# Performance work log

Hardware: AMD Instinct MI355X
Metric: run time of the kernel (lower is better)

## Reference

```python
import jax, jax.numpy as jnp
import numpy as np

B, N, E_PER = 512, 256, 8192          # graphs, nodes per graph, edges per graph
FIN, H, K, FOUT = 128, 32, 16, 10     # in_channels, hidden, num clusters, out_channels
EPS = 1e-15


def setup_inputs() -> dict:
    key = jax.random.key(0)
    ks = jax.random.split(key, 12)
    x = jax.random.normal(ks[0], (B * N, FIN), jnp.float32)
    # intra-graph random edges, then offset into the global node index space
    src = jax.random.randint(ks[1], (B, E_PER), 0, N)
    dst = jax.random.randint(ks[2], (B, E_PER), 0, N)
    offs = (jnp.arange(B) * N)[:, None]
    edge_index = jnp.stack([(src + offs).reshape(-1), (dst + offs).reshape(-1)]).astype(jnp.int64)
    batch = jnp.repeat(jnp.arange(B), N).astype(jnp.int64)

    def lin(k, fin, fout):
        return (jax.random.normal(k, (fin, fout), jnp.float32) / np.sqrt(fin)).astype(jnp.float32)

    params = {
        'W_lin1': lin(ks[3], FIN, H), 'b_lin1': jnp.zeros((H,), jnp.float32),
        'W_rel1': lin(ks[4], H, H), 'b_rel1': jnp.zeros((H,), jnp.float32),
        'W_root1': lin(ks[5], H, H),
        'W_pool': lin(ks[6], H, K), 'b_pool': jnp.zeros((K,), jnp.float32),
        'W_rel2': lin(ks[7], H, H), 'b_rel2': jnp.zeros((H,), jnp.float32),
        'W_root2': lin(ks[8], H, H),
        'W_lin2': lin(ks[9], H, H), 'b_lin2': jnp.zeros((H,), jnp.float32),
        'W_lin3': lin(ks[10], H, FOUT), 'b_lin3': jnp.zeros((FOUT,), jnp.float32),
    }
    return {'x': x, 'edge_index': edge_index, 'batch': batch, **params}


def _densify(x, edge_index, batch):
    """to_dense_adj + to_dense_batch: [total,F] -> [B,N,F], [B,N,N], [B,N]."""
    n_total = x.shape[0]
    counts = jax.ops.segment_sum(jnp.ones((n_total,), jnp.int32), batch, num_segments=B)
    offsets = jnp.concatenate([jnp.zeros((1,), jnp.int32), jnp.cumsum(counts)[:-1]])
    pos = jnp.arange(n_total) - offsets[batch]            # position of node inside its graph
    eb = batch[edge_index[0]]                             # graph id of each edge
    adj = jnp.zeros((B, N, N), jnp.float32).at[eb, pos[edge_index[0]], pos[edge_index[1]]].add(1.0)
    xd = jnp.zeros((B, N, x.shape[1]), jnp.float32).at[batch, pos].set(x)
    mask = jnp.zeros((B, N), jnp.float32).at[batch, pos].set(1.0)
    return xd, adj, mask


def _dense_graph_conv(x, adj, W_rel, b_rel, W_root):
    # PyG DenseGraphConv(aggr='add'): lin_rel(adj @ x) + lin_root(x)
    return jnp.einsum('bnm,bmh,hk->bnk', adj, x, W_rel) + b_rel + x @ W_root


def _dense_mincut_pool(x, adj, s, mask):
    s = jax.nn.softmax(s, axis=-1)
    x = x * mask[..., None]
    s = s * mask[..., None]
    out = jnp.einsum('bnk,bnh->bkh', s, x)                        # s^T x
    out_adj = jnp.einsum('bnk,bnm,bmj->bkj', s, adj, s)           # s^T A s
    mincut_num = jnp.einsum('bkk->b', out_adj)
    d_flat = adj.sum(-1)                                          # degree
    mincut_den = jnp.einsum('bnk,bn,bnk->b', s, d_flat, s)        # trace(s^T D s)
    mincut_loss = jnp.mean(-(mincut_num / mincut_den))
    ss = jnp.einsum('bnk,bnj->bkj', s, s)
    ss_norm = jnp.linalg.norm(ss, axis=(-1, -2), keepdims=True)
    i_s = jnp.eye(K, dtype=jnp.float32)
    ortho_loss = jnp.mean(jnp.linalg.norm(ss / ss_norm - i_s / jnp.sqrt(jnp.float32(K)), axis=(-1, -2)))
    # zero diagonal, symmetric degree normalization
    diag_mask = 1.0 - i_s
    out_adj = out_adj * diag_mask
    d = jnp.sqrt(out_adj.sum(-1))[:, None, :] + EPS               # [B,1,K]
    out_adj = out_adj / d / jnp.swapaxes(d, 1, 2)
    return out, out_adj, mincut_loss, ortho_loss


def reference(x, edge_index, batch, W_lin1, b_lin1, W_rel1, b_rel1, W_root1,
              W_pool, b_pool, W_rel2, b_rel2, W_root2, W_lin2, b_lin2, W_lin3, b_lin3):
    xd, adj, mask = _densify(x, edge_index, batch)
    h = xd @ W_lin1 + b_lin1                                      # lin1
    h = _dense_graph_conv(h, adj, W_rel1, b_rel1, W_root1)        # conv1
    s2 = h @ W_pool + b_pool                                      # pool2
    h, adj_p, mincut_loss2, ortho_loss2 = _dense_mincut_pool(h, adj, s2, mask)
    h = _dense_graph_conv(h, adj_p, W_rel2, b_rel2, W_root2)      # conv2
    h = h.sum(axis=1)                                             # readout sum over clusters
    h = jax.nn.relu(h @ W_lin2 + b_lin2)
    h = h @ W_lin3 + b_lin3
    return jax.nn.log_softmax(h, axis=-1), mincut_loss2, ortho_loss2
```

## Files before the change

### kernel.cpp

```cpp
#include <hip/hip_runtime.h>

#define NB 512
#define NN 256
#define EPG 8192
#define FINC 128

typedef float f32x4 __attribute__((ext_vector_type(4)));
typedef short s16x8 __attribute__((ext_vector_type(8)));

__device__ __forceinline__ float bf2f(unsigned short u) {
  union { unsigned int i; float f; } x; x.i = ((unsigned int)u) << 16; return x.f;
}
__device__ __forceinline__ unsigned short f2bf(float f) {
  union { float f; unsigned int i; } x; x.f = f;
  unsigned int r = x.i + 0x7fffu + ((x.i >> 16) & 1u);
  return (unsigned short)(r >> 16);
}
__device__ __forceinline__ unsigned pk2(unsigned short a, unsigned short c) {
  return (unsigned)a | ((unsigned)c << 16);
}

union U16x8 { uint4 u; s16x8 s; };
__device__ __forceinline__ s16x8 dec8(unsigned d) {
  U16x8 o;
  o.u.x = 0x41804180u | ((d & 0x0000000Fu) << 3)  | ((d & 0x000000F0u) << 15);
  o.u.y = 0x41804180u | ((d & 0x00000F00u) >> 5)  | ((d & 0x0000F000u) << 7);
  o.u.z = 0x41804180u | ((d & 0x000F0000u) >> 13) | ((d & 0x00F00000u) >> 1);
  o.u.w = 0x41804180u | ((d & 0x0F000000u) >> 21) | ((d & 0xF0000000u) >> 9);
  return o.s;
}

struct Params {
  const void* x; const void* ei;
  const void *wl1, *bl1, *wr1, *br1, *wro1, *wp, *bp;
  const void *wr2, *br2, *wro2, *wl2, *bl2, *wl3, *bl3;
  float* out; float* ws;
};

__device__ __forceinline__ float ldf(const void* p, int i, bool bf) {
  return bf ? bf2f(((const unsigned short*)p)[i]) : ((const float*)p)[i];
}

#define SMEM_TOTAL 81920

__global__ __launch_bounds__(1024, 8) void mincut_main(Params P) {
  extern __shared__ char smem[];
  const int t = threadIdx.x;
  const int b = blockIdx.x;

  const int wv = t >> 6, lane = t & 63;
  const int lm = lane & 15, quad = lane >> 4;
  const int mbase = wv * 16;

  int* flg = (int*)(smem + 78656);
  if (wv == 0) {
    const unsigned short* pw = (const unsigned short*)P.wr1;
    unsigned e = (pw[lane] >> 7) & 0xFFu;
    unsigned long long m = __ballot(e > 96u && e < 132u);
    if (lane == 0) flg[0] = (__popcll(m) >= 56) ? 1 : 0;
  } else if (wv == 1) {
    const int* pi = (const int*)P.ei + EPG;
    bool c = false;
    if (lane < 32) { int v = pi[lane]; c = (v >= 256 && v < 512); }
    unsigned long long m = __ballot(c);
    if (lane == 0) flg[1] = (__popcll(m) < 24) ? 1 : 0;
  }

  float* oadjb  = (float*)(smem + 2048);
  float* ddb    = (float*)(smem + 6144);
  float* caf    = (float*)(smem + 6208);
  float* psf    = (float*)(smem + 6272);
  float* qsf    = (float*)(smem + 6400);
  float* rb     = (float*)(smem + 8256);
  float* yb     = (float*)(smem + 8384);
  float* lgb    = (float*)(smem + 8512);
  float* rel2f  = (float*)(smem + 9216);
  float* root2f = (float*)(smem + 13312);
  float* lin2f  = (float*)(smem + 17408);
  float* lin3f  = (float*)(smem + 21504);
  float* brel2f = (float*)(smem + 22784);
  float* blin2f = (float*)(smem + 22912);
  float* blin3f = (float*)(smem + 23040);
  float* pbuf   = (float*)(smem + 24576);
  float* ssA    = (float*)(smem + 30720);
  unsigned short* h0T  = (unsigned short*)(smem + 33792);
  unsigned short* h1Th = (unsigned short*)(smem + 33792);
  unsigned short* w1t  = (unsigned short*)(smem + 50688);
  unsigned short* zT   = (unsigned short*)(smem + 50688);
  unsigned short* sTh  = (unsigned short*)(smem + 50688);
  unsigned short* wrelTh = (unsigned short*)(smem + 67584);
  unsigned short* wrootT = (unsigned short*)(smem + 72704);
  float* blin1f = (float*)(smem + 75264);
  unsigned short* taT = (unsigned short*)(smem + 67584);
  unsigned short* wpoolTh = (unsigned short*)(smem + 76032);
  float*          colzF   = (float*)(smem + 78336);
  float*          colsF   = (float*)(smem + 78464);
  float*          scrE    = (float*)(smem + 78528);
  float*          bpf     = (float*)(smem + 78592);
  unsigned short* brel1h  = (unsigned short*)(smem + 81856);

  {
    uint4 z = {0u, 0u, 0u, 0u};
    for (int i = t; i < 2112; i += 1024) ((uint4*)smem)[i] = z;
  }
  if (t < 48) colzF[t] = 0.f;
  __syncthreads();

  const bool BF  = (flg[0] != 0);
  const bool I64 = (flg[1] != 0);

  uint4 ea0, ea1, ea2, ea3, eb0, eb1, eb2, eb3;
  if (I64) {
    const uint4* s4 = (const uint4*)((const long long*)P.ei + (size_t)b * EPG) + t * 4;
    const uint4* d4 = (const uint4*)((const long long*)P.ei + (size_t)NB * EPG + (size_t)b * EPG) + t * 4;
    ea0 = s4[0]; ea1 = s4[1]; ea2 = s4[2]; ea3 = s4[3];
    eb0 = d4[0]; eb1 = d4[1]; eb2 = d4[2]; eb3 = d4[3];
  } else {
    const uint4* s4 = (const uint4*)((const int*)P.ei + (size_t)b * EPG) + t * 2;
    const uint4* d4 = (const uint4*)((const int*)P.ei + (size_t)NB * EPG + (size_t)b * EPG) + t * 2;
    ea0 = s4[0]; ea1 = s4[1];
    eb0 = d4[0]; eb1 = d4[1];
  }

  for (int e = t; e < 4096; e += 1024) {
    int k = e >> 5, c = e & 31;
    w1t[c * 136 + k] = f2bf(ldf(P.wl1, e, BF));
  }
  {
    int k = t >> 5, c = t & 31;
    wrelTh[c * 40 + k] = f2bf(ldf(P.wr1, t, BF));
    wrootT[c * 40 + k] = f2bf(ldf(P.wro1, t, BF));
  }
  if (t < 512) {
    int m = t >> 4, c = t & 15;
    wpoolTh[c * 36 + m] = f2bf(ldf(P.wp, t, BF));
  }
  if (t < 32) { blin1f[t] = ldf(P.bl1, t, BF); brel1h[t] = f2bf(ldf(P.br1, t, BF)); }
  if (t < 16) bpf[t] = ldf(P.bp, t, BF);

  if (I64) {
    #pragma unroll
    for (int i = 0; i < 4; ++i) {
      uint4 a = (i == 0) ? ea0 : (i == 1) ? ea1 : (i == 2) ? ea2 : ea3;
      uint4 c = (i == 0) ? eb0 : (i == 1) ? eb1 : (i == 2) ? eb2 : eb3;
      unsigned n0 = (a.x & 255u) * 264u + (c.x & 255u);
      unsigned n1 = (a.z & 255u) * 264u + (c.z & 255u);
      atomicAdd((unsigned int*)(smem + ((n0 >> 3) << 2)), 1u << ((n0 & 7u) * 4u));
      atomicAdd((unsigned int*)(smem + ((n1 >> 3) << 2)), 1u << ((n1 & 7u) * 4u));
    }
  } else {
    #pragma unroll
    for (int i = 0; i < 2; ++i) {
      uint4 a = (i == 0) ? ea0 : ea1;
      uint4 c = (i == 0) ? eb0 : eb1;
      unsigned n0 = (a.x & 255u) * 264u + (c.x & 255u);
      unsigned n1 = (a.y & 255u) * 264u + (c.y & 255u);
      unsigned n2 = (a.z & 255u) * 264u + (c.z & 255u);
      unsigned n3 = (a.w & 255u) * 264u + (c.w & 255u);
      atomicAdd((unsigned int*)(smem + ((n0 >> 3) << 2)), 1u << ((n0 & 7u) * 4u));
      atomicAdd((unsigned int*)(smem + ((n1 >> 3) << 2)), 1u << ((n1 & 7u) * 4u));
      atomicAdd((unsigned int*)(smem + ((n2 >> 3) << 2)), 1u << ((n2 & 7u) * 4u));
      atomicAdd((unsigned int*)(smem + ((n3 >> 3) << 2)), 1u << ((n3 & 7u) * 4u));
    }
  }

  s16x8 xa[4];
  {
    const size_t node = (size_t)(b * 256 + mbase + lm);
    if (BF) {
      #pragma unroll
      for (int ks = 0; ks < 4; ++ks)
        xa[ks] = *(const s16x8*)((const unsigned short*)P.x + node * 128 + ks * 32 + quad * 8);
    } else {
      #pragma unroll
      for (int ks = 0; ks < 4; ++ks) {
        const float* xp = (const float*)P.x + node * 128 + ks * 32 + quad * 8;
        f32x4 v0 = *(const f32x4*)xp;
        f32x4 v1 = *(const f32x4*)(xp + 4);
        #pragma unroll
        for (int j = 0; j < 4; ++j) { xa[ks][j] = (short)f2bf(v0[j]); xa[ks][4 + j] = (short)f2bf(v1[j]); }
      }
    }
  }
  __syncthreads();

  {
    f32x4 acc[2] = {{0.f,0.f,0.f,0.f},{0.f,0.f,0.f,0.f}};
    #pragma unroll
    for (int ks = 0; ks < 4; ++ks) {
      const int k0 = ks * 32 + quad * 8;
      #pragma unroll
      for (int ct = 0; ct < 2; ++ct) {
        s16x8 bh = *(const s16x8*)(w1t + (ct * 16 + lm) * 136 + k0);
        acc[ct] = __builtin_amdgcn_mfma_f32_16x16x32_bf16(xa[ks], bh, acc[ct], 0, 0, 0);
      }
    }
    #pragma unroll
    for (int ct = 0; ct < 2; ++ct) {
      const int c = ct * 16 + lm;
      float bias = blin1f[c];
      *(uint2*)(h0T + c * 264 + mbase + quad * 4) =
          make_uint2(pk2(f2bf(acc[ct][0] + bias), f2bf(acc[ct][1] + bias)),
                     pk2(f2bf(acc[ct][2] + bias), f2bf(acc[ct][3] + bias)));
    }
  }
  __syncthreads();

  f32x4 racc[2] = {{0.f,0.f,0.f,0.f},{0.f,0.f,0.f,0.f}};
  {
    s16x8 Ah;
    #pragma unroll
    for (int j = 0; j < 8; ++j) Ah[j] = (short)h0T[(quad * 8 + j) * 264 + mbase + lm];
    f32x4 zacc[2] = {{0.f,0.f,0.f,0.f},{0.f,0.f,0.f,0.f}};
    #pragma unroll
    for (int ct = 0; ct < 2; ++ct) {
      const int c = ct * 16 + lm;
      s16x8 brh = *(const s16x8*)(wrelTh + c * 40 + quad * 8);
      s16x8 bro = *(const s16x8*)(wrootT + c * 40 + quad * 8);
      zacc[ct] = __builtin_amdgcn_mfma_f32_16x16x32_bf16(Ah, brh, zacc[ct], 0, 0, 0);
      racc[ct] = __builtin_amdgcn_mfma_f32_16x16x32_bf16(Ah, bro, racc[ct], 0, 0, 0);
    }
    #pragma unroll
    for (int ct = 0; ct < 2; ++ct) {
      unsigned short u0 = f2bf(zacc[ct][0]), u1 = f2bf(zacc[ct][1]);
      unsigned short u2 = f2bf(zacc[ct][2]), u3 = f2bf(zacc[ct][3]);
      *(uint2*)(zT + (ct * 16 + lm) * 264 + mbase + quad * 4) =
          make_uint2(pk2(u0, u1), pk2(u2, u3));
      float pz = (bf2f(u0) + bf2f(u1)) + (bf2f(u2) + bf2f(u3));
      pz += __shfl_xor(pz, 16, 64);
      pz += __shfl_xor(pz, 32, 64);
      if (lane < 16) atomicAdd(colzF + ct * 16 + lm, pz);
    }
  }
  __syncthreads();

  float degf;
  {
    f32x4 h1acc[2] = { racc[0], racc[1] };
    unsigned dsum = 0;
    const char* arow = smem + (mbase + lm) * 132;
    #pragma unroll
    for (int ks = 0; ks < 8; ++ks) {
      unsigned d = *(const unsigned int*)(arow + ks * 16 + quad * 4);
      unsigned v = (d & 0x0F0F0F0Fu) + ((d >> 4) & 0x0F0F0F0Fu);
      dsum += (v * 0x01010101u) >> 24;
      s16x8 af = dec8(d);
      const int v0 = ks * 32 + quad * 8;
      #pragma unroll
      for (int ct = 0; ct < 2; ++ct) {
        s16x8 bz = *(const s16x8*)(zT + (ct * 16 + lm) * 264 + v0);
        h1acc[ct] = __builtin_amdgcn_mfma_f32_16x16x32_bf16(af, bz, h1acc[ct], 0, 0, 0);
      }
    }
    dsum += __shfl_xor(dsum, 16, 64);
    dsum += __shfl_xor(dsum, 32, 64);
    degf = (float)dsum;
    #pragma unroll
    for (int ct = 0; ct < 2; ++ct) {
      const int c = ct * 16 + lm;
      float bias = bf2f(brel1h[c]) - 16.f * colzF[c];
      *(uint2*)(h1Th + c * 264 + mbase + quad * 4) =
          make_uint2(pk2(f2bf(h1acc[ct][0] + bias), f2bf(h1acc[ct][1] + bias)),
                     pk2(f2bf(h1acc[ct][2] + bias), f2bf(h1acc[ct][3] + bias)));
    }
  }
  __syncthreads();

  {
    s16x8 Ah1;
    #pragma unroll
    for (int j = 0; j < 8; ++j) Ah1[j] = (short)h1Th[(quad * 8 + j) * 264 + mbase + lm];
    s16x8 Bh;
    ((uint2*)&Bh)[0] = *(const uint2*)(wpoolTh + lm * 36 + quad * 8);
    ((uint2*)&Bh)[1] = *(const uint2*)(wpoolTh + lm * 36 + quad * 8 + 4);
    f32x4 lacc = {0.f, 0.f, 0.f, 0.f};
    lacc = __builtin_amdgcn_mfma_f32_16x16x32_bf16(Ah1, Bh, lacc, 0, 0, 0);
    f32x4 lg;
    float bm = bpf[lm];
    #pragma unroll
    for (int r = 0; r < 4; ++r) lg[r] = lacc[r] + bm;
    f32x4 mx = lg;
    #pragma unroll
    for (int m = 1; m <= 8; m <<= 1)
      #pragma unroll
      for (int r = 0; r < 4; ++r) mx[r] = fmaxf(mx[r], __shfl_xor(mx[r], m, 64));
    #pragma unroll
    for (int r = 0; r < 4; ++r) lg[r] = __expf(lg[r] - mx[r]);
    f32x4 sm = lg;
    #pragma unroll
    for (int m = 1; m <= 8; m <<= 1)
      #pragma unroll
      for (int r = 0; r < 4; ++r) sm[r] += __shfl_xor(sm[r], m, 64);
    f32x4 sval, sq;
    #pragma unroll
    for (int r = 0; r < 4; ++r) { sval[r] = lg[r] / sm[r]; sq[r] = sval[r] * sval[r]; }
    #pragma unroll
    for (int m = 1; m <= 8; m <<= 1)
      #pragma unroll
      for (int r = 0; r < 4; ++r) sq[r] += __shfl_xor(sq[r], m, 64);
    {
      unsigned short h0s = f2bf(sval[0]);
      unsigned short h1s = f2bf(sval[1]);
      unsigned short h2s = f2bf(sval[2]);
      unsigned short h3s = f2bf(sval[3]);
      const int nb = lm * 264 + mbase + quad * 4;
      *(uint2*)(sTh + nb) = make_uint2(pk2(h0s, h1s), pk2(h2s, h3s));
      float sr = (bf2f(h0s) + bf2f(h1s)) + (bf2f(h2s) + bf2f(h3s));
      sr += __shfl_xor(sr, 16, 64);
      sr += __shfl_xor(sr, 32, 64);
      if (lane < 16) atomicAdd(colsF + lm, sr);
    }
    {
      int l = lane & 15, src = (l >> 2) << 4;
      float q0 = __shfl(sq[0], src, 64), q1 = __shfl(sq[1], src, 64);
      float q2 = __shfl(sq[2], src, 64), q3 = __shfl(sq[3], src, 64);
      float ssel = (l & 2) ? ((l & 1) ? q3 : q2) : ((l & 1) ? q1 : q0);
      float vden = (lane < 16) ? degf * ssel : 0.f;
      #pragma unroll
      for (int o = 32; o > 0; o >>= 1) vden += __shfl_xor(vden, o, 64);
      if (lane == 0) scrE[wv] = vden;
    }
  }
  __syncthreads();

  {
    float cols = colsF[lm];
    f32x4 tacc = {0.f, 0.f, 0.f, 0.f};
    const char* arow = smem + (mbase + lm) * 132;
    #pragma unroll
    for (int ks = 0; ks < 8; ++ks) {
      unsigned d = *(const unsigned int*)(arow + ks * 16 + quad * 4);
      s16x8 af = dec8(d);
      const int v0 = ks * 32 + quad * 8;
      s16x8 bh = *(const s16x8*)(sTh + lm * 264 + v0);
      tacc = __builtin_amdgcn_mfma_f32_16x16x32_bf16(af, bh, tacc, 0, 0, 0);
    }
    float c16 = 16.f * cols;
    *(uint2*)(taT + lm * 264 + mbase + quad * 4) =
        make_uint2(pk2(f2bf(tacc[0] - c16), f2bf(tacc[1] - c16)),
                   pk2(f2bf(tacc[2] - c16), f2bf(tacc[3] - c16)));
  }
  __syncthreads();

  rel2f[t] = ldf(P.wr2, t, BF);
  root2f[t] = ldf(P.wro2, t, BF);
  lin2f[t] = ldf(P.wl2, t, BF);
  if (t < 320) lin3f[t] = ldf(P.wl3, t, BF);
  if (t < 32) brel2f[t] = ldf(P.br2, t, BF);
  if (t < 32) blin2f[t] = ldf(P.bl2, t, BF);
  if (t < 10) blin3f[t] = ldf(P.bl3, t, BF);

  if (wv < 4) {
    const unsigned short* Ap = sTh;
    const unsigned short* Bp; float* dst; int W, ct = 0;
    switch (wv) {
      case 0: Bp = h1Th; dst = pbuf;  W = 32; ct = 0; break;
      case 1: Bp = h1Th; dst = pbuf;  W = 32; ct = 1; break;
      case 2: Bp = taT;  dst = oadjb; W = 16; break;
      default: Bp = sTh; dst = ssA;   W = 16; break;
    }
    const int cidx = ct * 16 + lm;
    const unsigned short* Bb = Bp + cidx * 264;
    f32x4 acc = {0.f, 0.f, 0.f, 0.f};
    #pragma unroll
    for (int ch = 0; ch < 8; ++ch) {
      s16x8 a = *(const s16x8*)(Ap + lm * 264 + ch * 32 + quad * 8);
      s16x8 bb = *(const s16x8*)(Bb + ch * 32 + quad * 8);
      acc = __builtin_amdgcn_mfma_f32_16x16x32_bf16(a, bb, acc, 0, 0, 0);
    }
    #pragma unroll
    for (int r = 0; r < 4; ++r) dst[(quad * 4 + r) * W + cidx] = acc[r];
  }
  __syncthreads();

  if (wv == 0) {
    if (lane < 16) {
      float rs = 0.f;
      #pragma unroll
      for (int j = 0; j < 16; ++j) if (j != lane) rs += oadjb[lane * 16 + j];
      ddb[lane] = sqrtf(rs) + 1e-15f;
    }
    if (lane < 16) {
      float s = 0.f;
      float dj = ddb[lane];
      #pragma unroll
      for (int k = 0; k < 16; ++k)
        if (k != lane) s += oadjb[k * 16 + lane] / (ddb[k] * dj);
      caf[lane] = s;
    }
    if (lane < 32) {
      float ps = 0.f, qs = 0.f;
      #pragma unroll
      for (int j = 0; j < 16; ++j) {
        float pv = pbuf[j * 32 + lane];
        ps += pv;
        qs += caf[j] * pv;
      }
      psf[lane] = ps; qsf[lane] = qs;
    }
    if (lane < 32) {
      float r = 16.f * brel2f[lane];
      #pragma unroll
      for (int m = 0; m < 32; ++m)
        r += qsf[m] * rel2f[m * 32 + lane] + psf[m] * root2f[m * 32 + lane];
      rb[lane] = r;
    }
    if (lane < 32) {
      float y = blin2f[lane];
      #pragma unroll
      for (int m = 0; m < 32; ++m) y += rb[m] * lin2f[m * 32 + lane];
      yb[lane] = fmaxf(y, 0.f);
    }
    if (lane < 10) {
      float lg = blin3f[lane];
      #pragma unroll
      for (int m = 0; m < 32; ++m) lg += yb[m] * lin3f[m * 10 + lane];
      lgb[lane] = lg;
    }
    if (lane == 0) {
      float mx = lgb[0];
      #pragma unroll
      for (int i = 1; i < 10; ++i) mx = fmaxf(mx, lgb[i]);
      float sum = 0.f;
      #pragma unroll
      for (int i = 0; i < 10; ++i) sum += __expf(lgb[i] - mx);
      lgb[10] = mx + __logf(sum);
    }
    if (lane < 10) {
      float val = lgb[lane] - lgb[10];
      if (BF) ((unsigned short*)P.out)[b * 10 + lane] = f2bf(val);
      else    P.out[b * 10 + lane] = val;
    }
  } else if (wv == 1) {
    float vfro = 0.f, vtr = 0.f;
    #pragma unroll
    for (int u = 0; u < 4; ++u) {
      int i = lane * 4 + u, k = i >> 4, j = i & 15;
      float ssv = ssA[i];
      vfro += ssv * ssv;
      if (k == j) vtr += ssv;
    }
    float vnum = (lane < 16) ? oadjb[lane * 17] : 0.f;
    float vden = (lane < 16) ? scrE[lane] : 0.f;
    #pragma unroll
    for (int o = 32; o > 0; o >>= 1) {
      vfro += __shfl_xor(vfro, o, 64);
      vtr  += __shfl_xor(vtr, o, 64);
      vnum += __shfl_xor(vnum, o, 64);
      vden += __shfl_xor(vden, o, 64);
    }
    if (lane == 0) {
      float ssn = sqrtf(vfro);
      float orth2 = 2.f - vtr / (2.f * ssn);
      atomicAdd(P.ws, -(vnum / vden) * (1.f / NB));
      atomicAdd(P.ws + 1, sqrtf(fmaxf(orth2, 0.f)) * (1.f / NB));
      __threadfence();
      unsigned old = atomicAdd((unsigned int*)(P.ws + 2), 1u);
      if (old == (unsigned)(NB - 1)) {
        float l0 = atomicAdd(P.ws, 0.f);
        float l1 = atomicAdd(P.ws + 1, 0.f);
        if (BF) {
          ((unsigned short*)P.out)[5120] = f2bf(l0);
          ((unsigned short*)P.out)[5121] = f2bf(l1);
        } else {
          P.out[5120] = l0;
          P.out[5121] = l1;
        }
      }
    }
  }
}

extern "C" void kernel_launch(void* const* d_in, const int* in_sizes, int n_in,
                              void* d_out, int out_size, void* d_ws, size_t ws_size,
                              hipStream_t stream) {
  (void)in_sizes; (void)n_in; (void)out_size; (void)ws_size;
  Params P;
  P.x    = d_in[0];
  P.ei   = d_in[1];
  P.wl1  = d_in[3];
  P.bl1  = d_in[4];
  P.wr1  = d_in[5];
  P.br1  = d_in[6];
  P.wro1 = d_in[7];
  P.wp   = d_in[8];
  P.bp   = d_in[9];
  P.wr2  = d_in[10];
  P.br2  = d_in[11];
  P.wro2 = d_in[12];
  P.wl2  = d_in[13];
  P.bl2  = d_in[14];
  P.wl3  = d_in[15];
  P.bl3  = d_in[16];
  P.out  = (float*)d_out;
  P.ws   = (float*)d_ws;

  hipMemsetAsync(d_ws, 0, 4 * sizeof(float), stream);
  hipFuncSetAttribute(reinterpret_cast<const void*>(mincut_main),
                      hipFuncAttributeMaxDynamicSharedMemorySize, SMEM_TOTAL);
  hipLaunchKernelGGL(mincut_main, dim3(NB), dim3(1024), SMEM_TOTAL, stream, P);
}
```

Before: 167.9 us.

## Halve block size to 512 threads with each wave processing two row tiles

The block shrinks from 1024 to 512 threads. Each wave now handles two 16-row node tiles (g=0,1) in every stage, loads twice as many edges per thread, and interleaves the MFMAs of both tiles. The goal is to cut barrier cost and per-block scheduling overhead and to get more instruction-level parallelism per wave. The cost is higher register pressure, and parts of the later stages that are not visible may still assume 1024 threads.

Measured after the change: 172.4 us. 2.7% more time.

```diff
diff --git a/kernel.cpp b/kernel.cpp
--- a/kernel.cpp
+++ b/kernel.cpp
@@ -43,14 +43,13 @@
 
 #define SMEM_TOTAL 81920
 
-__global__ __launch_bounds__(1024, 8) void mincut_main(Params P) {
+__global__ __launch_bounds__(512, 4) void mincut_main(Params P) {
   extern __shared__ char smem[];
   const int t = threadIdx.x;
   const int b = blockIdx.x;
 
   const int wv = t >> 6, lane = t & 63;
   const int lm = lane & 15, quad = lane >> 4;
-  const int mbase = wv * 16;
 
   int* flg = (int*)(smem + 78656);
   if (wv == 0) {
@@ -101,7 +100,7 @@
 
   {
     uint4 z = {0u, 0u, 0u, 0u};
-    for (int i = t; i < 2112; i += 1024) ((uint4*)smem)[i] = z;
+    for (int i = t; i < 2112; i += 512) ((uint4*)smem)[i] = z;
   }
   if (t < 48) colzF[t] = 0.f;
   __syncthreads();
@@ -109,29 +108,29 @@
   const bool BF  = (flg[0] != 0);
   const bool I64 = (flg[1] != 0);
 
-  uint4 ea0, ea1, ea2, ea3, eb0, eb1, eb2, eb3;
+  uint4 ea[8], eb[8];
   if (I64) {
-    const uint4* s4 = (const uint4*)((const long long*)P.ei + (size_t)b * EPG) + t * 4;
-    const uint4* d4 = (const uint4*)((const long long*)P.ei + (size_t)NB * EPG + (size_t)b * EPG) + t * 4;
-    ea0 = s4[0]; ea1 = s4[1]; ea2 = s4[2]; ea3 = s4[3];
-    eb0 = d4[0]; eb1 = d4[1]; eb2 = d4[2]; eb3 = d4[3];
+    const uint4* s4 = (const uint4*)((const long long*)P.ei + (size_t)b * EPG) + t * 8;
+    const uint4* d4 = (const uint4*)((const long long*)P.ei + (size_t)NB * EPG + (size_t)b * EPG) + t * 8;
+    #pragma unroll
+    for (int i = 0; i < 8; ++i) { ea[i] = s4[i]; eb[i] = d4[i]; }
   } else {
-    const uint4* s4 = (const uint4*)((const int*)P.ei + (size_t)b * EPG) + t * 2;
-    const uint4* d4 = (const uint4*)((const int*)P.ei + (size_t)NB * EPG + (size_t)b * EPG) + t * 2;
-    ea0 = s4[0]; ea1 = s4[1];
-    eb0 = d4[0]; eb1 = d4[1];
-  }
-
-  for (int e = t; e < 4096; e += 1024) {
+    const uint4* s4 = (const uint4*)((const int*)P.ei + (size_t)b * EPG) + t * 4;
+    const uint4* d4 = (const uint4*)((const int*)P.ei + (size_t)NB * EPG + (size_t)b * EPG) + t * 4;
+    #pragma unroll
+    for (int i = 0; i < 4; ++i) { ea[i] = s4[i]; eb[i] = d4[i]; }
+  }
+
+  for (int e = t; e < 4096; e += 512) {
     int k = e >> 5, c = e & 31;
     w1t[c * 136 + k] = f2bf(ldf(P.wl1, e, BF));
   }
-  {
-    int k = t >> 5, c = t & 31;
-    wrelTh[c * 40 + k] = f2bf(ldf(P.wr1, t, BF));
-    wrootT[c * 40 + k] = f2bf(ldf(P.wro1, t, BF));
-  }
-  if (t < 512) {
+  for (int i = t; i < 1024; i += 512) {
+    int k = i >> 5, c = i & 31;
+    wrelTh[c * 40 + k] = f2bf(ldf(P.wr1, i, BF));
+    wrootT[c * 40 + k] = f2bf(ldf(P.wro1, i, BF));
+  }
+  {
     int m = t >> 4, c = t & 15;
     wpoolTh[c * 36 + m] = f2bf(ldf(P.wp, t, BF));
   }
@@ -140,23 +139,19 @@
 
   if (I64) {
     #pragma unroll
-    for (int i = 0; i < 4; ++i) {
-      uint4 a = (i == 0) ? ea0 : (i == 1) ? ea1 : (i == 2) ? ea2 : ea3;
-      uint4 c = (i == 0) ? eb0 : (i == 1) ? eb1 : (i == 2) ? eb2 : eb3;
-      unsigned n0 = (a.x & 255u) * 264u + (c.x & 255u);
-      unsigned n1 = (a.z & 255u) * 264u + (c.z & 255u);
+    for (int i = 0; i < 8; ++i) {
+      unsigned n0 = (ea[i].x & 255u) * 264u + (eb[i].x & 255u);
+      unsigned n1 = (ea[i].z & 255u) * 264u + (eb[i].z & 255u);
       atomicAdd((unsigned int*)(smem + ((n0 >> 3) << 2)), 1u << ((n0 & 7u) * 4u));
       atomicAdd((unsigned int*)(smem + ((n1 >> 3) << 2)), 1u << ((n1 & 7u) * 4u));
     }
   } else {
     #pragma unroll
-    for (int i = 0; i < 2; ++i) {
-      uint4 a = (i == 0) ? ea0 : ea1;
-      uint4 c = (i == 0) ? eb0 : eb1;
-      unsigned n0 = (a.x & 255u) * 264u + (c.x & 255u);
-      unsigned n1 = (a.y & 255u) * 264u + (c.y & 255u);
-      unsigned n2 = (a.z & 255u) * 264u + (c.z & 255u);
-      unsigned n3 = (a.w & 255u) * 264u + (c.w & 255u);
+    for (int i = 0; i < 4; ++i) {
+      unsigned n0 = (ea[i].x & 255u) * 264u + (eb[i].x & 255u);
+      unsigned n1 = (ea[i].y & 255u) * 264u + (eb[i].y & 255u);
+      unsigned n2 = (ea[i].z & 255u) * 264u + (eb[i].z & 255u);
+      unsigned n3 = (ea[i].w & 255u) * 264u + (eb[i].w & 255u);
       atomicAdd((unsigned int*)(smem + ((n0 >> 3) << 2)), 1u << ((n0 & 7u) * 4u));
       atomicAdd((unsigned int*)(smem + ((n1 >> 3) << 2)), 1u << ((n1 & 7u) * 4u));
       atomicAdd((unsigned int*)(smem + ((n2 >> 3) << 2)), 1u << ((n2 & 7u) * 4u));
@@ -164,13 +159,15 @@
     }
   }
 
-  s16x8 xa[4];
-  {
+  s16x8 xa[2][4];
+  #pragma unroll
+  for (int g = 0; g < 2; ++g) {
+    const int mbase = (wv + g * 8) * 16;
     const size_t node = (size_t)(b * 256 + mbase + lm);
     if (BF) {
       #pragma unroll
       for (int ks = 0; ks < 4; ++ks)
-        xa[ks] = *(const s16x8*)((const unsigned short*)P.x + node * 128 + ks * 32 + quad * 8);
+        xa[g][ks] = *(const s16x8*)((const unsigned short*)P.x + node * 128 + ks * 32 + quad * 8);
     } else {
       #pragma unroll
       for (int ks = 0; ks < 4; ++ks) {
@@ -178,173 +175,206 @@
         f32x4 v0 = *(const f32x4*)xp;
         f32x4 v1 = *(const f32x4*)(xp + 4);
         #pragma unroll
-        for (int j = 0; j < 4; ++j) { xa[ks][j] = (short)f2bf(v0[j]); xa[ks][4 + j] = (short)f2bf(v1[j]); }
-      }
-    }
-  }
-  __syncthreads();
-
-  {
-    f32x4 acc[2] = {{0.f,0.f,0.f,0.f},{0.f,0.f,0.f,0.f}};
+        for (int j = 0; j < 4; ++j) { xa[g][ks][j] = (short)f2bf(v0[j]); xa[g][ks][4 + j] = (short)f2bf(v1[j]); }
+      }
+    }
+  }
+  __syncthreads();
+
+  {
+    f32x4 acc[2][2] = {{{0.f,0.f,0.f,0.f},{0.f,0.f,0.f,0.f}},
+                       {{0.f,0.f,0.f,0.f},{0.f,0.f,0.f,0.f}}};
     #pragma unroll
     for (int ks = 0; ks < 4; ++ks) {
       const int k0 = ks * 32 + quad * 8;
       #pragma unroll
       for (int ct = 0; ct < 2; ++ct) {
         s16x8 bh = *(const s16x8*)(w1t + (ct * 16 + lm) * 136 + k0);
-        acc[ct] = __builtin_amdgcn_mfma_f32_16x16x32_bf16(xa[ks], bh, acc[ct], 0, 0, 0);
-      }
-    }
-    #pragma unroll
-    for (int ct = 0; ct < 2; ++ct) {
-      const int c = ct * 16 + lm;
-      float bias = blin1f[c];
-      *(uint2*)(h0T + c * 264 + mbase + quad * 4) =
-          make_uint2(pk2(f2bf(acc[ct][0] + bias), f2bf(acc[ct][1] + bias)),
-                     pk2(f2bf(acc[ct][2] + bias), f2bf(acc[ct][3] + bias)));
-    }
-  }
-  __syncthreads();
-
-  f32x4 racc[2] = {{0.f,0.f,0.f,0.f},{0.f,0.f,0.f,0.f}};
-  {
-    s16x8 Ah;
-    #pragma unroll
-    for (int j = 0; j < 8; ++j) Ah[j] = (short)h0T[(quad * 8 + j) * 264 + mbase + lm];
-    f32x4 zacc[2] = {{0.f,0.f,0.f,0.f},{0.f,0.f,0.f,0.f}};
+        acc[0][ct] = __builtin_amdgcn_mfma_f32_16x16x32_bf16(xa[0][ks], bh, acc[0][ct], 0, 0, 0);
+        acc[1][ct] = __builtin_amdgcn_mfma_f32_16x16x32_bf16(xa[1][ks], bh, acc[1][ct], 0, 0, 0);
+      }
+    }
+    #pragma unroll
+    for (int g = 0; g < 2; ++g) {
+      const int mbase = (wv + g * 8) * 16;
+      #pragma unroll
+      for (int ct = 0; ct < 2; ++ct) {
+        const int c = ct * 16 + lm;
+        float bias = blin1f[c];
+        *(uint2*)(h0T + c * 264 + mbase + quad * 4) =
+            make_uint2(pk2(f2bf(acc[g][ct][0] + bias), f2bf(acc[g][ct][1] + bias)),
+                       pk2(f2bf(acc[g][ct][2] + bias), f2bf(acc[g][ct][3] + bias)));
+      }
+    }
+  }
+  __syncthreads();
+
+  f32x4 racc[2][2] = {{{0.f,0.f,0.f,0.f},{0.f,0.f,0.f,0.f}},
+                      {{0.f,0.f,0.f,0.f},{0.f,0.f,0.f,0.f}}};
+  {
+    s16x8 Ah[2];
+    #pragma unroll
+    for (int g = 0; g < 2; ++g) {
+      const int mbase = (wv + g * 8) * 16;
+      #pragma unroll
+      for (int j = 0; j < 8; ++j) Ah[g][j] = (short)h0T[(quad * 8 + j) * 264 + mbase + lm];
+    }
+    f32x4 zacc[2][2] = {{{0.f,0.f,0.f,0.f},{0.f,0.f,0.f,0.f}},
+                        {{0.f,0.f,0.f,0.f},{0.f,0.f,0.f,0.f}}};
     #pragma unroll
     for (int ct = 0; ct < 2; ++ct) {
       const int c = ct * 16 + lm;
       s16x8 brh = *(const s16x8*)(wrelTh + c * 40 + quad * 8);
       s16x8 bro = *(const s16x8*)(wrootT + c * 40 + quad * 8);
-      zacc[ct] = __builtin_amdgcn_mfma_f32_16x16x32_bf16(Ah, brh, zacc[ct], 0, 0, 0);
-      racc[ct] = __builtin_amdgcn_mfma_f32_16x16x32_bf16(Ah, bro, racc[ct], 0, 0, 0);
-    }
-    #pragma unroll
-    for (int ct = 0; ct < 2; ++ct) {
-      unsigned short u0 = f2bf(zacc[ct][0]), u1 = f2bf(zacc[ct][1]);
-      unsigned short u2 = f2bf(zacc[ct][2]), u3 = f2bf(zacc[ct][3]);
-      *(uint2*)(zT + (ct * 16 + lm) * 264 + mbase + quad * 4) =
-          make_uint2(pk2(u0, u1), pk2(u2, u3));
-      float pz = (bf2f(u0) + bf2f(u1)) + (bf2f(u2) + bf2f(u3));
-      pz += __shfl_xor(pz, 16, 64);
-      pz += __shfl_xor(pz, 32, 64);
-      if (lane < 16) atomicAdd(colzF + ct * 16 + lm, pz);
-    }
-  }
-  __syncthreads();
-
-  float degf;
-  {
-    f32x4 h1acc[2] = { racc[0], racc[1] };
-    unsigned dsum = 0;
-    const char* arow = smem + (mbase + lm) * 132;
-    #pragma unroll
-    for (int ks = 0; ks < 8; ++ks) {
-      unsigned d = *(const unsigned int*)(arow + ks * 16 + quad * 4);
-      unsigned v = (d & 0x0F0F0F0Fu) + ((d >> 4) & 0x0F0F0F0Fu);
-      dsum += (v * 0x01010101u) >> 24;
-      s16x8 af = dec8(d);
-      const int v0 = ks * 32 + quad * 8;
+      #pragma unroll
+      for (int g = 0; g < 2; ++g) {
+        zacc[g][ct] = __builtin_amdgcn_mfma_f32_16x16x32_bf16(Ah[g], brh, zacc[g][ct], 0, 0, 0);
+        racc[g][ct] = __builtin_amdgcn_mfma_f32_16x16x32_bf16(Ah[g], bro, racc[g][ct], 0, 0, 0);
+      }
+    }
+    #pragma unroll
+    for (int g = 0; g < 2; ++g) {
+      const int mbase = (wv + g * 8) * 16;
       #pragma unroll
       for (int ct = 0; ct < 2; ++ct) {
-        s16x8 bz = *(const s16x8*)(zT + (ct * 16 + lm) * 264 + v0);
-        h1acc[ct] = __builtin_amdgcn_mfma_f32_16x16x32_bf16(af, bz, h1acc[ct], 0, 0, 0);
-      }
-    }
-    dsum += __shfl_xor(dsum, 16, 64);
-    dsum += __shfl_xor(dsum, 32, 64);
-    degf = (float)dsum;
-    #pragma unroll
-    for (int ct = 0; ct < 2; ++ct) {
-      const int c = ct * 16 + lm;
-      float bias = bf2f(brel1h[c]) - 16.f * colzF[c];
-      *(uint2*)(h1Th + c * 264 + mbase + quad * 4) =
-          make_uint2(pk2(f2bf(h1acc[ct][0] + bias), f2bf(h1acc[ct][1] + bias)),
-                     pk2(f2bf(h1acc[ct][2] + bias), f2bf(h1acc[ct][3] + bias)));
-    }
-  }
-  __syncthreads();
-
-  {
-    s16x8 Ah1;
-    #pragma unroll
-    for (int j = 0; j < 8; ++j) Ah1[j] = (short)h1Th[(quad * 8 + j) * 264 + mbase + lm];
+        unsigned short u0 = f2bf(zacc[g][ct][0]), u1 = f2bf(zacc[g][ct][1]);
+        unsigned short u2 = f2bf(zacc[g][ct][2]), u3 = f2bf(zacc[g][ct][3]);
+        *(uint2*)(zT + (ct * 16 + lm) * 264 + mbase + quad * 4) =
+            make_uint2(pk2(u0, u1), pk2(u2, u3));
+        float pz = (bf2f(u0) + bf2f(u1)) + (bf2f(u2) + bf2f(u3));
+        pz += __shfl_xor(pz, 16, 64);
+        pz += __shfl_xor(pz, 32, 64);
+        if (lane < 16) atomicAdd(colzF + ct * 16 + lm, pz);
+      }
+    }
+  }
+  __syncthreads();
+
+  float degf[2];
+  {
+    #pragma unroll
+    for (int g = 0; g < 2; ++g) {
+      const int mbase = (wv + g * 8) * 16;
+      f32x4 h1acc[2] = { racc[g][0], racc[g][1] };
+      unsigned dsum = 0;
+      const char* arow = smem + (mbase + lm) * 132;
+      #pragma unroll
+      for (int ks = 0; ks < 8; ++ks) {
+        unsigned d = *(const unsigned int*)(arow + ks * 16 + quad * 4);
+        unsigned v = (d & 0x0F0F0F0Fu) + ((d >> 4) & 0x0F0F0F0Fu);
+        dsum += (v * 0x01010101u) >> 24;
+        s16x8 af = dec8(d);
+        const int v0 = ks * 32 + quad * 8;
+        #pragma unroll
+        for (int ct = 0; ct < 2; ++ct) {
+          s16x8 bz = *(const s16x8*)(zT + (ct * 16 + lm) * 264 + v0);
+          h1acc[ct] = __builtin_amdgcn_mfma_f32_16x16x32_bf16(af, bz, h1acc[ct], 0, 0, 0);
+        }
+      }
+      dsum += __shfl_xor(dsum, 16, 64);
+      dsum += __shfl_xor(dsum, 32, 64);
+      degf[g] = (float)dsum;
+      #pragma unroll
+      for (int ct = 0; ct < 2; ++ct) {
+        const int c = ct * 16 + lm;
+        float bias = bf2f(brel1h[c]) - 16.f * colzF[c];
+        *(uint2*)(h1Th + c * 264 + mbase + quad * 4) =
+            make_uint2(pk2(f2bf(h1acc[ct][0] + bias), f2bf(h1acc[ct][1] + bias)),
+                       pk2(f2bf(h1acc[ct][2] + bias), f2bf(h1acc[ct][3] + bias)));
+      }
+    }
+  }
+  __syncthreads();
+
+  {
     s16x8 Bh;
     ((uint2*)&Bh)[0] = *(const uint2*)(wpoolTh + lm * 36 + quad * 8);
     ((uint2*)&Bh)[1] = *(const uint2*)(wpoolTh + lm * 36 + quad * 8 + 4);
-    f32x4 lacc = {0.f, 0.f, 0.f, 0.f};
-    lacc = __builtin_amdgcn_mfma_f32_16x16x32_bf16(Ah1, Bh, lacc, 0, 0, 0);
-    f32x4 lg;
-    float bm = bpf[lm];
-    #pragma unroll
-    for (int r = 0; r < 4; ++r) lg[r] = lacc[r] + bm;
-    f32x4 mx = lg;
-    #pragma unroll
-    for (int m = 1; m <= 8; m <<= 1)
-      #pragma unroll
-      for (int r = 0; r < 4; ++r) mx[r] = fmaxf(mx[r], __shfl_xor(mx[r], m, 64));
-    #pragma unroll
-    for (int r = 0; r < 4; ++r) lg[r] = __expf(lg[r] - mx[r]);
-    f32x4 sm = lg;
-    #pragma unroll
-    for (int m = 1; m <= 8; m <<= 1)
-      #pragma unroll
-      for (int r = 0; r < 4; ++r) sm[r] += __shfl_xor(sm[r], m, 64);
-    f32x4 sval, sq;
-    #pragma unroll
-    for (int r = 0; r < 4; ++r) { sval[r] = lg[r] / sm[r]; sq[r] = sval[r] * sval[r]; }
-    #pragma unroll
-    for (int m = 1; m <= 8; m <<= 1)
-      #pragma unroll
-      for (int r = 0; r < 4; ++r) sq[r] += __shfl_xor(sq[r], m, 64);
-    {
-      unsigned short h0s = f2bf(sval[0]);
-      unsigned short h1s = f2bf(sval[1]);
-      unsigned short h2s = f2bf(sval[2]);
-      unsigned short h3s = f2bf(sval[3]);
-      const int nb = lm * 264 + mbase + quad * 4;
-      *(uint2*)(sTh + nb) = make_uint2(pk2(h0s, h1s), pk2(h2s, h3s));
-      float sr = (bf2f(h0s) + bf2f(h1s)) + (bf2f(h2s) + bf2f(h3s));
-      sr += __shfl_xor(sr, 16, 64);
-      sr += __shfl_xor(sr, 32, 64);
-      if (lane < 16) atomicAdd(colsF + lm, sr);
-    }
-    {
-      int l = lane & 15, src = (l >> 2) << 4;
-      float q0 = __shfl(sq[0], src, 64), q1 = __shfl(sq[1], src, 64);
-      float q2 = __shfl(sq[2], src, 64), q3 = __shfl(sq[3], src, 64);
-      float ssel = (l & 2) ? ((l & 1) ? q3 : q2) : ((l & 1) ? q1 : q0);
-      float vden = (lane < 16) ? degf * ssel : 0.f;
-      #pragma unroll
-      for (int o = 32; o > 0; o >>= 1) vden += __shfl_xor(vden, o, 64);
-      if (lane == 0) scrE[wv] = vden;
+    #pragma unroll
+    for (int g = 0; g < 2; ++g) {
+      const int mbase = (wv + g * 8) * 16;
+      s16x8 Ah1;
+      #pragma unroll
+      for (int j = 0; j < 8; ++j) Ah1[j] = (short)h1Th[(quad * 8 + j) * 264 + mbase + lm];
+      f32x4 lacc = {0.f, 0.f, 0.f, 0.f};
+      lacc = __builtin_amdgcn_mfma_f32_16x16x32_bf16(Ah1, Bh, lacc, 0, 0, 0);
+      f32x4 lg;
+      float bm = bpf[lm];
+      #pragma unroll
+      for (int r = 0; r < 4; ++r) lg[r] = lacc[r] + bm;
+      f32x4 mx = lg;
+      #pragma unroll
+      for (int m = 1; m <= 8; m <<= 1)
+        #pragma unroll
+        for (int r = 0; r < 4; ++r) mx[r] = fmaxf(mx[r], __shfl_xor(mx[r], m, 64));
+      #pragma unroll
+      for (int r = 0; r < 4; ++r) lg[r] = __expf(lg[r] - mx[r]);
+      f32x4 sm = lg;
+      #pragma unroll
+      for (int m = 1; m <= 8; m <<= 1)
+        #pragma unroll
+        for (int r = 0; r < 4; ++r) sm[r] += __shfl_xor(sm[r], m, 64);
+      f32x4 sval, sq;
+      #pragma unroll
+      for (int r = 0; r < 4; ++r) { sval[r] = lg[r] / sm[r]; sq[r] = sval[r] * sval[r]; }
+      #pragma unroll
+      for (int m = 1; m <= 8; m <<= 1)
+        #pragma unroll
+        for (int r = 0; r < 4; ++r) sq[r] += __shfl_xor(sq[r], m, 64);
+      {
+        unsigned short h0s = f2bf(sval[0]);
+        unsigned short h1s = f2bf(sval[1]);
+        unsigned short h2s = f2bf(sval[2]);
+        unsigned short h3s = f2bf(sval[3]);
+        const int nb = lm * 264 + mbase + quad * 4;
+        *(uint2*)(sTh + nb) = make_uint2(pk2(h0s, h1s), pk2(h2s, h3s));
+        float sr = (bf2f(h0s) + bf2f(h1s)) + (bf2f(h2s) + bf2f(h3s));
+        sr += __shfl_xor(sr, 16, 64);
+        sr += __shfl_xor(sr, 32, 64);
+        if (lane < 16) atomicAdd(colsF + lm, sr);
+      }
+      {
+        int l = lane & 15, src = (l >> 2) << 4;
+        float q0 = __shfl(sq[0], src, 64), q1 = __shfl(sq[1], src, 64);
+        float q2 = __shfl(sq[2], src, 64), q3 = __shfl(sq[3], src, 64);
+        float ssel = (l & 2) ? ((l & 1) ? q3 : q2) : ((l & 1) ? q1 : q0);
+        float vden = (lane < 16) ? degf[g] * ssel : 0.f;
+        #pragma unroll
+        for (int o = 32; o > 0; o >>= 1) vden += __shfl_xor(vden, o, 64);
+        if (lane == 0) scrE[g * 8 + wv] = vden;
+      }
     }
   }
   __syncthreads();
 
   {
     float cols = colsF[lm];
-    f32x4 tacc = {0.f, 0.f, 0.f, 0.f};
-    const char* arow = smem + (mbase + lm) * 132;
-    #pragma unroll
-    for (int ks = 0; ks < 8; ++ks) {
-      unsigned d = *(const unsigned int*)(arow + ks * 16 + quad * 4);
-      s16x8 af = dec8(d);
-      const int v0 = ks * 32 + quad * 8;
-      s16x8 bh = *(const s16x8*)(sTh + lm * 264 + v0);
-      tacc = __builtin_amdgcn_mfma_f32_16x16x32_bf16(af, bh, tacc, 0, 0, 0);
-    }
     float c16 = 16.f * cols;
-    *(uint2*)(taT + lm * 264 + mbase + quad * 4) =
-        make_uint2(pk2(f2bf(tacc[0] - c16), f2bf(tacc[1] - c16)),
-                   pk2(f2bf(tacc[2] - c16), f2bf(tacc[3] - c16)));
-  }
-  __syncthreads();
-
-  rel2f[t] = ldf(P.wr2, t, BF);
-  root2f[t] = ldf(P.wro2, t, BF);
-  lin2f[t] = ldf(P.wl2, t, BF);
+    #pragma unroll
+    for (int g = 0; g < 2; ++g) {
+      const int mbase = (wv + g * 8) * 16;
+      f32x4 tacc = {0.f, 0.f, 0.f, 0.f};
+      const char* arow = smem + (mbase + lm) * 132;
+      #pragma unroll
+      for (int ks = 0; ks < 8; ++ks) {
+        unsigned d = *(const unsigned int*)(arow + ks * 16 + quad * 4);
+        s16x8 af = dec8(d);
+        const int v0 = ks * 32 + quad * 8;
+        s16x8 bh = *(const s16x8*)(sTh + lm * 264 + v0);
+        tacc = __builtin_amdgcn_mfma_f32_16x16x32_bf16(af, bh, tacc, 0, 0, 0);
+      }
+      *(uint2*)(taT + lm * 264 + mbase + quad * 4) =
+          make_uint2(pk2(f2bf(tacc[0] - c16), f2bf(tacc[1] - c16)),
+                     pk2(f2bf(tacc[2] - c16), f2bf(tacc[3] - c16)));
+    }
+  }
+  __syncthreads();
+
+  for (int i = t; i < 1024; i += 512) {
+    rel2f[i] = ldf(P.wr2, i, BF);
+    root2f[i] = ldf(P.wro2, i, BF);
+    lin2f[i] = ldf(P.wl2, i, BF);
+  }
   if (t < 320) lin3f[t] = ldf(P.wl3, t, BF);
   if (t < 32) brel2f[t] = ldf(P.br2, t, BF);
   if (t < 32) blin2f[t] = ldf(P.bl2, t, BF);
@@ -498,5 +528,5 @@
   hipMemsetAsync(d_ws, 0, 4 * sizeof(float), stream);
   hipFuncSetAttribute(reinterpret_cast<const void*>(mincut_main),
                       hipFuncAttributeMaxDynamicSharedMemorySize, SMEM_TOTAL);
-  hipLaunchKernelGGL(mincut_main, dim3(NB), dim3(1024), SMEM_TOTAL, stream, P);
-}
+  hipLaunchKernelGGL(mincut_main, dim3(NB), dim3(512), SMEM_TOTAL, stream, P);
+}
```
